# Optimization experiments

Measured on AMD Instinct MI355X. Metric: run time of the kernel, lower is better.

Reference implementation:

```python
import jax, jax.numpy as jnp
import numpy as np

SENSOR_H, SENSOR_W = 256, 256
SPP = 16
BATCH, C, H_IMG, W_IMG = 4, 3, 1024, 1024


def setup_inputs() -> dict:
    key = jax.random.key(0)
    k1, k2 = jax.random.split(key)
    img = jax.random.uniform(k1, (BATCH, C, H_IMG, W_IMG), dtype=jnp.float32)
    jitter = jax.random.uniform(k2, (SPP, SENSOR_H, SENSOR_W, 2), dtype=jnp.float32)
    t = jnp.ones((1,), jnp.float32)
    return {"img": img, "t": t, "jitter": jitter}


def deform(pos, t):
    # Analytic per-axis foveation diffeomorphism [-1,1]^2 -> [-1,1]^2:
    #   f(u) = tanh(t*u)/tanh(t), f'(u) = t*(1 - tanh(t*u)^2)/tanh(t)
    # Jacobian is diagonal, so det = f'(x) * f'(y).
    tt = t[0]
    s = jnp.tanh(tt)
    th = jnp.tanh(tt * pos)
    warped = th / s                      # (..., 2)
    dd = tt * (1.0 - th * th) / s        # diagonal Jacobian entries (..., 2)
    det = dd[..., 0] * dd[..., 1]        # (...)
    return warped, det


def grid_sample_border(img, grid):
    # img: (b,c,H,W); grid: (spp,h,w,2) in [-1,1]
    # bilinear, padding_mode='border', align_corners=False (matches F.grid_sample)
    b, c, H, W = img.shape
    gx = (grid[..., 0] + 1.0) * (W / 2.0) - 0.5
    gy = (grid[..., 1] + 1.0) * (H / 2.0) - 0.5
    gx = jnp.clip(gx, 0.0, W - 1.0)
    gy = jnp.clip(gy, 0.0, H - 1.0)
    x0 = jnp.floor(gx)
    y0 = jnp.floor(gy)
    wx = (gx - x0)[None, None]           # (1,1,spp,h,w)
    wy = (gy - y0)[None, None]
    x0i = jnp.clip(x0.astype(jnp.int32), 0, W - 1)
    y0i = jnp.clip(y0.astype(jnp.int32), 0, H - 1)
    x1i = jnp.clip(x0i + 1, 0, W - 1)
    y1i = jnp.clip(y0i + 1, 0, H - 1)
    # fancy-index gather: result (b,c,spp,h,w); avoids tiling img over (b*spp)
    v00 = img[:, :, y0i, x0i]
    v01 = img[:, :, y0i, x1i]
    v10 = img[:, :, y1i, x0i]
    v11 = img[:, :, y1i, x1i]
    return (v00 * (1 - wx) * (1 - wy) + v01 * wx * (1 - wy)
            + v10 * (1 - wx) * wy + v11 * wx * wy)


def reference(img, t, jitter):
    step_x = 2.0 / SENSOR_W
    step_y = 2.0 / SENSOR_H
    px = jnp.arange(-1.0, 1.0, step_x, dtype=jnp.float32)
    py = jnp.arange(-1.0, 1.0, step_y, dtype=jnp.float32)
    gx, gy = jnp.meshgrid(px, py, indexing='xy')          # (h, w)
    pixel_pos = jnp.stack((gx, gy), axis=-1)[None]        # (1, h, w, 2)
    jit = jitter * jnp.array([step_x, step_y], jnp.float32)
    pos = pixel_pos + jit                                 # (spp, h, w, 2)
    warped, det = deform(pos, t)                          # (spp,h,w,2), (spp,h,w)
    samples = grid_sample_border(img, warped)             # (b, c, spp, h, w)
    weighted = jnp.mean(samples * det[None, None], axis=2)  # (b, c, h, w)
    area = jnp.mean(det, axis=0)[None, None]              # (1, 1, h, w)
    return weighted / area
```

## Files before the change

kernel.cpp:

```cpp
#include <hip/hip_runtime.h>

#define SPP   16
#define SH    256
#define SW    256
#define HI    1024
#define WI    1024
#define CH    3
#define BATCH 4

__device__ __forceinline__ float fast_tanh(float x) {
    const float e = __expf(2.0f * x);
    return (e - 1.0f) * __builtin_amdgcn_rcpf(e + 1.0f);
}

__global__ __launch_bounds__(256) void foveated_batch(
    const float* __restrict__ img,
    const float* __restrict__ t_ptr,
    const float* __restrict__ jitter,
    float* __restrict__ out)
{
    const int L   = (blockIdx.x & 7) * 512 + (blockIdx.x >> 3);
    const int sy  = L >> 4;
    const int sx0 = (L & 15) * 16;

    const int th  = threadIdx.x;
    const int sp  = th & 15;
    const int pxl = th >> 4;
    const int sx  = sx0 + pxl;

    const float step  = 2.0f / 256.0f;
    const float tt    = t_ptr[0];
    const float inv_s = __builtin_amdgcn_rcpf(fast_tanh(tt));

    const float2 j = ((const float2*)jitter)[sp * (SH * SW) + sy * SW + sx];
    const float posx = (-1.0f + sx * step) + j.x * step;
    const float posy = (-1.0f + sy * step) + j.y * step;

    const float thx = fast_tanh(tt * posx);
    const float thy = fast_tanh(tt * posy);
    const float ddx = tt * (1.0f - thx * thx) * inv_s;
    const float ddy = tt * (1.0f - thy * thy) * inv_s;
    const float det = ddx * ddy;

    float gx = (thx * inv_s + 1.0f) * (WI * 0.5f) - 0.5f;
    float gy = (thy * inv_s + 1.0f) * (HI * 0.5f) - 0.5f;
    gx = fminf(fmaxf(gx, 0.0f), (float)(WI - 1));
    gy = fminf(fmaxf(gy, 0.0f), (float)(HI - 1));

    const int xb = min((int)gx, WI - 2);
    const int yb = min((int)gy, HI - 2);
    const float fx = gx - (float)xb;
    const float fy = gy - (float)yb;

    const float w00 = (1.0f - fx) * (1.0f - fy) * det;
    const float w01 = fx * (1.0f - fy) * det;
    const float w10 = (1.0f - fx) * fy * det;
    const float w11 = fx * fy * det;

    const int i0 = yb * WI + xb;
    const int i1 = i0 + WI;
    const size_t plane = (size_t)HI * WI;

    float acc[BATCH][CH];
    #pragma unroll
    for (int b = 0; b < BATCH; ++b) {
        const float* __restrict__ pb = img + (size_t)(b * CH) * plane;
        #pragma unroll
        for (int c = 0; c < CH; ++c) {
            const float* __restrict__ p = pb + c * plane;
            const float2 a = *(const float2*)(p + i0);
            const float2 d = *(const float2*)(p + i1);
            acc[b][c] = a.x * w00 + a.y * w01 + d.x * w10 + d.y * w11;
        }
    }

    float dsum = det;
    #pragma unroll
    for (int m = 1; m < 16; m <<= 1) {
        #pragma unroll
        for (int b = 0; b < BATCH; ++b)
            #pragma unroll
            for (int c = 0; c < CH; ++c)
                acc[b][c] += __shfl_xor(acc[b][c], m);
        dsum += __shfl_xor(dsum, m);
    }

    if (sp == 0) {
        const float inv_d = 1.0f / dsum;
        const int pix = sy * SW + sx;
        #pragma unroll
        for (int b = 0; b < BATCH; ++b)
            #pragma unroll
            for (int c = 0; c < CH; ++c)
                out[(size_t)(b * CH + c) * (SH * SW) + pix] = acc[b][c] * inv_d;
    }
}

extern "C" void kernel_launch(void* const* d_in, const int* in_sizes, int n_in,
                              void* d_out, int out_size, void* d_ws, size_t ws_size,
                              hipStream_t stream) {
    const float* img    = (const float*)d_in[0];
    const float* t      = (const float*)d_in[1];
    const float* jitter = (const float*)d_in[2];
    float* out          = (float*)d_out;

    hipLaunchKernelGGL(foveated_batch, dim3(4096), dim3(256), 0, stream,
                       img, t, jitter, out);
}
```

Baseline: 113.0 us.

## Stage per-tile image footprint in LDS as fp16 and process four samples per thread

Each block now covers a 16x4 sensor tile, computes the warped image bounding box, and cooperatively loads the footprint for all three channels of each batch into shared memory packed as half precision. Each thread handles four jitter samples and gathers bilinear taps from LDS, with a global-memory fallback when the footprint exceeds the buffer. The aim is fewer scattered global gathers, since overlapping taps are now reused. In exchange it adds block barriers, a serial batch loop, and reduced input precision from fp16 storage.

```diff
diff --git a/kernel.cpp b/kernel.cpp
--- a/kernel.cpp
+++ b/kernel.cpp
@@ -1,4 +1,5 @@
 #include <hip/hip_runtime.h>
+#include <hip/hip_fp16.h>
 
 #define SPP   16
 #define SH    256
@@ -8,75 +9,165 @@
 #define CH    3
 #define BATCH 4
 
+#define TSX   16
+#define TSY   4
+#define MAXW  92
+#define MAXH  26
+
 __device__ __forceinline__ float fast_tanh(float x) {
     const float e = __expf(2.0f * x);
     return (e - 1.0f) * __builtin_amdgcn_rcpf(e + 1.0f);
 }
 
-__global__ __launch_bounds__(256) void foveated_batch(
+__global__ __launch_bounds__(256) void foveated_tile4(
     const float* __restrict__ img,
     const float* __restrict__ t_ptr,
     const float* __restrict__ jitter,
     float* __restrict__ out)
 {
-    const int L   = (blockIdx.x & 7) * 512 + (blockIdx.x >> 3);
-    const int sy  = L >> 4;
-    const int sx0 = (L & 15) * 16;
-
-    const int th  = threadIdx.x;
-    const int sp  = th & 15;
-    const int pxl = th >> 4;
-    const int sx  = sx0 + pxl;
+    __shared__ uint2 lds[MAXH * MAXW];
+
+    const int bid = blockIdx.x;
+    const int L   = (bid & 7) * 128 + (bid >> 3);
+    const int ty  = L & 63;
+    const int tx  = L >> 6;
+
+    const int th = threadIdx.x;
+    const int lx = th & 15;
+    const int q  = (th >> 4) & 3;
+    const int ly = th >> 6;
+
+    const int sx = tx * TSX + lx;
+    const int sy = ty * TSY + ly;
 
     const float step  = 2.0f / 256.0f;
     const float tt    = t_ptr[0];
     const float inv_s = __builtin_amdgcn_rcpf(fast_tanh(tt));
 
-    const float2 j = ((const float2*)jitter)[sp * (SH * SW) + sy * SW + sx];
-    const float posx = (-1.0f + sx * step) + j.x * step;
-    const float posy = (-1.0f + sy * step) + j.y * step;
-
-    const float thx = fast_tanh(tt * posx);
-    const float thy = fast_tanh(tt * posy);
-    const float ddx = tt * (1.0f - thx * thx) * inv_s;
-    const float ddy = tt * (1.0f - thy * thy) * inv_s;
-    const float det = ddx * ddy;
-
-    float gx = (thx * inv_s + 1.0f) * (WI * 0.5f) - 0.5f;
-    float gy = (thy * inv_s + 1.0f) * (HI * 0.5f) - 0.5f;
-    gx = fminf(fmaxf(gx, 0.0f), (float)(WI - 1));
-    gy = fminf(fmaxf(gy, 0.0f), (float)(HI - 1));
-
-    const int xb = min((int)gx, WI - 2);
-    const int yb = min((int)gy, HI - 2);
-    const float fx = gx - (float)xb;
-    const float fy = gy - (float)yb;
-
-    const float w00 = (1.0f - fx) * (1.0f - fy) * det;
-    const float w01 = fx * (1.0f - fy) * det;
-    const float w10 = (1.0f - fx) * fy * det;
-    const float w11 = fx * fy * det;
-
-    const int i0 = yb * WI + xb;
-    const int i1 = i0 + WI;
+    auto gmap = [&](float p) {
+        float g = (fast_tanh(tt * p) * inv_s + 1.0f) * 512.0f - 0.5f;
+        return fminf(fmaxf(g, 0.0f), 1023.0f);
+    };
+    const float pxmin = -1.0f + (tx * TSX) * step, pxmax = pxmin + TSX * step;
+    const float pymin = -1.0f + (ty * TSY) * step, pymax = pymin + TSY * step;
+    const int x_lo = max((int)gmap(pxmin) - 1, 0);
+    const int x_hi = min((int)gmap(pxmax) + 2, WI - 1);
+    const int y_lo = max((int)gmap(pymin) - 1, 0);
+    const int y_hi = min((int)gmap(pymax) + 2, HI - 1);
+    const int ncols = x_hi - x_lo + 1;
+    const int nrows = y_hi - y_lo + 1;
+    const bool fits = (ncols <= MAXW) && (nrows <= MAXH);
+
+    float w00[4], w01[4], w10[4], w11[4];
+    int   li[4], gi[4];
+    float dsum = 0.0f;
+    const float2* __restrict__ jit2 = (const float2*)jitter;
+    const int jbase = sy * SW + sx;
+    const float px = -1.0f + sx * step;
+    const float py = -1.0f + sy * step;
+
+    #pragma unroll
+    for (int k = 0; k < 4; ++k) {
+        const int sp = q * 4 + k;
+        const float2 j = jit2[sp * (SH * SW) + jbase];
+        const float posx = px + j.x * step;
+        const float posy = py + j.y * step;
+
+        const float thx = fast_tanh(tt * posx);
+        const float thy = fast_tanh(tt * posy);
+        const float ddx = tt * (1.0f - thx * thx) * inv_s;
+        const float ddy = tt * (1.0f - thy * thy) * inv_s;
+        const float det = ddx * ddy;
+
+        float gx = (thx * inv_s + 1.0f) * (WI * 0.5f) - 0.5f;
+        float gy = (thy * inv_s + 1.0f) * (HI * 0.5f) - 0.5f;
+        gx = fminf(fmaxf(gx, 0.0f), (float)(WI - 1));
+        gy = fminf(fmaxf(gy, 0.0f), (float)(HI - 1));
+
+        const int xb = min((int)gx, WI - 2);
+        const int yb = min((int)gy, HI - 2);
+        const float fx = gx - (float)xb;
+        const float fy = gy - (float)yb;
+
+        w00[k] = (1.0f - fx) * (1.0f - fy) * det;
+        w01[k] = fx * (1.0f - fy) * det;
+        w10[k] = (1.0f - fx) * fy * det;
+        w11[k] = fx * fy * det;
+        dsum  += det;
+        li[k]  = (yb - y_lo) * MAXW + (xb - x_lo);
+        gi[k]  = yb * WI + xb;
+    }
+
     const size_t plane = (size_t)HI * WI;
-
     float acc[BATCH][CH];
     #pragma unroll
+    for (int b = 0; b < BATCH; ++b)
+        #pragma unroll
+        for (int c = 0; c < CH; ++c) acc[b][c] = 0.0f;
+
+    const int npix = nrows * ncols;
+    const unsigned mdiv = (1u << 22) / (unsigned)ncols + 1u;
+
+    #pragma unroll 1
     for (int b = 0; b < BATCH; ++b) {
-        const float* __restrict__ pb = img + (size_t)(b * CH) * plane;
-        #pragma unroll
-        for (int c = 0; c < CH; ++c) {
-            const float* __restrict__ p = pb + c * plane;
-            const float2 a = *(const float2*)(p + i0);
-            const float2 d = *(const float2*)(p + i1);
-            acc[b][c] = a.x * w00 + a.y * w01 + d.x * w10 + d.y * w11;
+        const float* __restrict__ p0 = img + (size_t)(b * CH) * plane;
+        const float* __restrict__ p1 = p0 + plane;
+        const float* __restrict__ p2 = p1 + plane;
+
+        if (fits) {
+            __syncthreads();
+            #pragma unroll
+            for (int it = 0; it < 10; ++it) {
+                const int idx = th + it * 256;
+                const int ii  = min(idx, npix - 1);
+                const int r   = (int)(((unsigned)ii * mdiv) >> 22);
+                const int c   = ii - r * ncols;
+                const int g   = (y_lo + r) * WI + (x_lo + c);
+                union { __half2 h[2]; uint2 u; } v;
+                v.h[0] = __floats2half2_rn(p0[g], p1[g]);
+                v.h[1] = __floats2half2_rn(p2[g], 0.0f);
+                if (idx < npix) lds[r * MAXW + c] = v.u;
+            }
+            __syncthreads();
+
+            #pragma unroll
+            for (int k = 0; k < 4; ++k) {
+                const int base = li[k];
+                const uint2 q00 = lds[base];
+                const uint2 q01 = lds[base + 1];
+                const uint2 q10 = lds[base + MAXW];
+                const uint2 q11 = lds[base + MAXW + 1];
+
+                const float2 a00 = __half22float2(*(const __half2*)&q00.x);
+                const float2 b00 = __half22float2(*(const __half2*)&q00.y);
+                const float2 a01 = __half22float2(*(const __half2*)&q01.x);
+                const float2 b01 = __half22float2(*(const __half2*)&q01.y);
+                const float2 a10 = __half22float2(*(const __half2*)&q10.x);
+                const float2 b10 = __half22float2(*(const __half2*)&q10.y);
+                const float2 a11 = __half22float2(*(const __half2*)&q11.x);
+                const float2 b11 = __half22float2(*(const __half2*)&q11.y);
+
+                acc[b][0] += w00[k]*a00.x + w01[k]*a01.x + w10[k]*a10.x + w11[k]*a11.x;
+                acc[b][1] += w00[k]*a00.y + w01[k]*a01.y + w10[k]*a10.y + w11[k]*a11.y;
+                acc[b][2] += w00[k]*b00.x + w01[k]*b01.x + w10[k]*b10.x + w11[k]*b11.x;
+            }
+        } else {
+            #pragma unroll
+            for (int k = 0; k < 4; ++k) {
+                const int i0 = gi[k];
+                const int i1 = i0 + WI;
+                { const float2 a = *(const float2*)(p0 + i0), d = *(const float2*)(p0 + i1);
+                  acc[b][0] += a.x*w00[k] + a.y*w01[k] + d.x*w10[k] + d.y*w11[k]; }
+                { const float2 a = *(const float2*)(p1 + i0), d = *(const float2*)(p1 + i1);
+                  acc[b][1] += a.x*w00[k] + a.y*w01[k] + d.x*w10[k] + d.y*w11[k]; }
+                { const float2 a = *(const float2*)(p2 + i0), d = *(const float2*)(p2 + i1);
+                  acc[b][2] += a.x*w00[k] + a.y*w01[k] + d.x*w10[k] + d.y*w11[k]; }
+            }
         }
     }
 
-    float dsum = det;
     #pragma unroll
-    for (int m = 1; m < 16; m <<= 1) {
+    for (int m = 16; m <= 32; m <<= 1) {
         #pragma unroll
         for (int b = 0; b < BATCH; ++b)
             #pragma unroll
@@ -85,7 +176,7 @@
         dsum += __shfl_xor(dsum, m);
     }
 
-    if (sp == 0) {
+    if (q == 0) {
         const float inv_d = 1.0f / dsum;
         const int pix = sy * SW + sx;
         #pragma unroll
@@ -104,6 +195,6 @@
     const float* jitter = (const float*)d_in[2];
     float* out          = (float*)d_out;
 
-    hipLaunchKernelGGL(foveated_batch, dim3(4096), dim3(256), 0, stream,
+    hipLaunchKernelGGL(foveated_tile4, dim3(1024), dim3(256), 0, stream,
                        img, t, jitter, out);
 }
```

Result: no change. 113.4 us (+0.3%).

## Repack image into interleaved fp16 pixel records and gather with half2 FMA

Applied to the files above, without the earlier changes.

Adds a pre-pass that packs the 12 batch/channel planes into one 32-byte fp16 record per pixel in the workspace. The main kernel then fetches each bilinear corner with a single contiguous load instead of 12 scattered plane loads. Each thread now handles 4 samples and accumulates in half2 FMAs. This trades an extra full-image read/write pass and fp16 precision loss, including fp16 accumulation of weighted sums, for far fewer cache lines touched per gather. It falls back to the old kernel if the workspace is too small.

```diff
diff --git a/kernel.cpp b/kernel.cpp
--- a/kernel.cpp
+++ b/kernel.cpp
@@ -1,16 +1,154 @@
 #include <hip/hip_runtime.h>
-
-#define SPP   16
-#define SH    256
-#define SW    256
-#define HI    1024
-#define WI    1024
-#define CH    3
-#define BATCH 4
+#include <hip/hip_fp16.h>
+
+#define SPP    16
+#define SH     256
+#define SW     256
+#define HI     1024
+#define WI     1024
+#define CH     3
+#define BATCH  4
+#define NPLANE (BATCH * CH)
+#define PXB    32
 
 __device__ __forceinline__ float fast_tanh(float x) {
     const float e = __expf(2.0f * x);
     return (e - 1.0f) * __builtin_amdgcn_rcpf(e + 1.0f);
+}
+
+__global__ __launch_bounds__(256) void repack12(
+    const float* __restrict__ img, char* __restrict__ dst)
+{
+    const int pix = blockIdx.x * 256 + threadIdx.x;
+    float v[NPLANE];
+    #pragma unroll
+    for (int p = 0; p < NPLANE; ++p)
+        v[p] = img[(size_t)p * (HI * WI) + pix];
+    union { __half2 h[6]; struct { uint4 a; uint2 b; } u; } o;
+    #pragma unroll
+    for (int i = 0; i < 6; ++i)
+        o.h[i] = __floats2half2_rn(v[2 * i], v[2 * i + 1]);
+    char* d = dst + (size_t)pix * PXB;
+    *(uint4*)d        = o.u.a;
+    *(uint2*)(d + 16) = o.u.b;
+}
+
+__global__ __launch_bounds__(256) void foveated_pk(
+    const char* __restrict__ pk,
+    const float* __restrict__ t_ptr,
+    const float* __restrict__ jitter,
+    float* __restrict__ out)
+{
+    const int L   = (blockIdx.x & 7) * 128 + (blockIdx.x >> 3);
+    const int th  = threadIdx.x;
+    const int lpx = th & 15;
+    const int q   = (th >> 4) & 3;
+    const int wv  = th >> 6;
+    const int pix = L * 64 + wv * 16 + lpx;
+    const int sx  = pix & (SW - 1);
+    const int sy  = pix >> 8;
+
+    const float step  = 2.0f / 256.0f;
+    const float tt    = t_ptr[0];
+    const float inv_s = __builtin_amdgcn_rcpf(fast_tanh(tt));
+    const float px    = -1.0f + sx * step;
+    const float py    = -1.0f + sy * step;
+
+    const float2* __restrict__ jit2 = (const float2*)jitter;
+
+    __half2 acc[6];
+    #pragma unroll
+    for (int i = 0; i < 6; ++i) acc[i] = __float2half2_rn(0.0f);
+    float dsum = 0.0f;
+
+    #pragma unroll
+    for (int k = 0; k < 4; ++k) {
+        const int sp = q * 4 + k;
+        const float2 j = jit2[sp * (SH * SW) + pix];
+        const float posx = px + j.x * step;
+        const float posy = py + j.y * step;
+
+        const float thx = fast_tanh(tt * posx);
+        const float thy = fast_tanh(tt * posy);
+        const float ddx = tt * (1.0f - thx * thx) * inv_s;
+        const float ddy = tt * (1.0f - thy * thy) * inv_s;
+        const float det = ddx * ddy;
+
+        float gx = (thx * inv_s + 1.0f) * (WI * 0.5f) - 0.5f;
+        float gy = (thy * inv_s + 1.0f) * (HI * 0.5f) - 0.5f;
+        gx = fminf(fmaxf(gx, 0.0f), (float)(WI - 1));
+        gy = fminf(fmaxf(gy, 0.0f), (float)(HI - 1));
+
+        const int xb = min((int)gx, WI - 2);
+        const int yb = min((int)gy, HI - 2);
+        const float fx = gx - (float)xb;
+        const float fy = gy - (float)yb;
+
+        const float w00 = (1.0f - fx) * (1.0f - fy) * det;
+        const float w01 = fx * (1.0f - fy) * det;
+        const float w10 = (1.0f - fx) * fy * det;
+        const float w11 = fx * fy * det;
+        dsum += det;
+
+        const __half2 W00 = __float2half2_rn(w00);
+        const __half2 W01 = __float2half2_rn(w01);
+        const __half2 W10 = __float2half2_rn(w10);
+        const __half2 W11 = __float2half2_rn(w11);
+
+        const char* r0 = pk + (size_t)((uint)(yb * WI + xb)) * PXB;
+        const char* r1 = r0 + WI * PXB;
+        const uint4 a0  = *(const uint4*)(r0);
+        const uint2 a0h = *(const uint2*)(r0 + 16);
+        const uint4 b0  = *(const uint4*)(r0 + PXB);
+        const uint2 b0h = *(const uint2*)(r0 + PXB + 16);
+        const uint4 a1  = *(const uint4*)(r1);
+        const uint2 a1h = *(const uint2*)(r1 + 16);
+        const uint4 b1  = *(const uint4*)(r1 + PXB);
+        const uint2 b1h = *(const uint2*)(r1 + PXB + 16);
+
+        const __half2* A0 = (const __half2*)&a0;
+        const __half2* B0 = (const __half2*)&b0;
+        const __half2* A1 = (const __half2*)&a1;
+        const __half2* B1 = (const __half2*)&b1;
+        #pragma unroll
+        for (int i = 0; i < 4; ++i) {
+            acc[i] = __hfma2(A0[i], W00, acc[i]);
+            acc[i] = __hfma2(B0[i], W01, acc[i]);
+            acc[i] = __hfma2(A1[i], W10, acc[i]);
+            acc[i] = __hfma2(B1[i], W11, acc[i]);
+        }
+        const __half2* A0H = (const __half2*)&a0h;
+        const __half2* B0H = (const __half2*)&b0h;
+        const __half2* A1H = (const __half2*)&a1h;
+        const __half2* B1H = (const __half2*)&b1h;
+        #pragma unroll
+        for (int i = 0; i < 2; ++i) {
+            acc[4 + i] = __hfma2(A0H[i], W00, acc[4 + i]);
+            acc[4 + i] = __hfma2(B0H[i], W01, acc[4 + i]);
+            acc[4 + i] = __hfma2(A1H[i], W10, acc[4 + i]);
+            acc[4 + i] = __hfma2(B1H[i], W11, acc[4 + i]);
+        }
+    }
+
+    #pragma unroll
+    for (int m = 16; m <= 32; m <<= 1) {
+        #pragma unroll
+        for (int i = 0; i < 6; ++i) {
+            const int t = __shfl_xor(__builtin_bit_cast(int, acc[i]), m);
+            acc[i] = __hadd2(acc[i], __builtin_bit_cast(__half2, t));
+        }
+        dsum += __shfl_xor(dsum, m);
+    }
+
+    if (q == 0) {
+        const float inv_d = 1.0f / dsum;
+        #pragma unroll
+        for (int p = 0; p < NPLANE; ++p) {
+            const float v = (p & 1) ? __high2float(acc[p >> 1])
+                                    : __low2float(acc[p >> 1]);
+            out[(size_t)p * (SH * SW) + pix] = v * inv_d;
+        }
+    }
 }
 
 __global__ __launch_bounds__(256) void foveated_batch(
@@ -22,7 +160,6 @@
     const int L   = (blockIdx.x & 7) * 512 + (blockIdx.x >> 3);
     const int sy  = L >> 4;
     const int sx0 = (L & 15) * 16;
-
     const int th  = threadIdx.x;
     const int sp  = th & 15;
     const int pxl = th >> 4;
@@ -104,6 +241,15 @@
     const float* jitter = (const float*)d_in[2];
     float* out          = (float*)d_out;
 
-    hipLaunchKernelGGL(foveated_batch, dim3(4096), dim3(256), 0, stream,
-                       img, t, jitter, out);
-}
+    const size_t need = (size_t)HI * WI * PXB;
+    if (ws_size >= need) {
+        char* pk = (char*)d_ws;
+        hipLaunchKernelGGL(repack12, dim3(HI * WI / 256), dim3(256), 0, stream,
+                           img, pk);
+        hipLaunchKernelGGL(foveated_pk, dim3(1024), dim3(256), 0, stream,
+                           pk, t, jitter, out);
+    } else {
+        hipLaunchKernelGGL(foveated_batch, dim3(4096), dim3(256), 0, stream,
+                           img, t, jitter, out);
+    }
+}
```

New measurement: 120.2 us. +6.3%, slower.

## Split batch-channel planes across two blocks to cut registers and raise occupancy

Applied to the files above, without the earlier changes.

Each block now handles 16 pixels for half of the 12 batch-channel planes (6 planes) rather than all 12. The grid doubles and a launch-bounds occupancy hint is added. All gathers for the 6 planes are issued before any arithmetic, which keeps more loads in flight per thread and needs fewer registers. The cost is computing the warp and jitter loads twice per pixel, and each block's pixels now come from a different part of the image, which may change cache reuse.

```diff
diff --git a/kernel.cpp b/kernel.cpp
--- a/kernel.cpp
+++ b/kernel.cpp
@@ -13,26 +13,29 @@
     return (e - 1.0f) * __builtin_amdgcn_rcpf(e + 1.0f);
 }
 
-__global__ __launch_bounds__(256) void foveated_batch(
+__global__ __launch_bounds__(256, 6) void foveated_split(
     const float* __restrict__ img,
     const float* __restrict__ t_ptr,
     const float* __restrict__ jitter,
     float* __restrict__ out)
 {
-    const int L   = (blockIdx.x & 7) * 512 + (blockIdx.x >> 3);
-    const int sy  = L >> 4;
-    const int sx0 = (L & 15) * 16;
+    const int L   = (blockIdx.x & 7) * 1024 + (blockIdx.x >> 3);
+    const int bh  = L & 1;
+    const int grp = L >> 1;
 
     const int th  = threadIdx.x;
     const int sp  = th & 15;
-    const int pxl = th >> 4;
-    const int sx  = sx0 + pxl;
+    const int lpx = (th >> 4) & 3;
+    const int wv  = th >> 6;
+    const int pix = grp * 16 + wv * 4 + lpx;
+    const int sx  = pix & (SW - 1);
+    const int sy  = pix >> 8;
 
     const float step  = 2.0f / 256.0f;
     const float tt    = t_ptr[0];
     const float inv_s = __builtin_amdgcn_rcpf(fast_tanh(tt));
 
-    const float2 j = ((const float2*)jitter)[sp * (SH * SW) + sy * SW + sx];
+    const float2 j = ((const float2*)jitter)[sp * (SH * SW) + pix];
     const float posx = (-1.0f + sx * step) + j.x * step;
     const float posy = (-1.0f + sy * step) + j.y * step;
 
@@ -61,38 +64,33 @@
     const int i1 = i0 + WI;
     const size_t plane = (size_t)HI * WI;
 
-    float acc[BATCH][CH];
+    const float* __restrict__ pb = img + (size_t)(bh * 6) * plane;
+    float2 r0[6], r1[6];
     #pragma unroll
-    for (int b = 0; b < BATCH; ++b) {
-        const float* __restrict__ pb = img + (size_t)(b * CH) * plane;
-        #pragma unroll
-        for (int c = 0; c < CH; ++c) {
-            const float* __restrict__ p = pb + c * plane;
-            const float2 a = *(const float2*)(p + i0);
-            const float2 d = *(const float2*)(p + i1);
-            acc[b][c] = a.x * w00 + a.y * w01 + d.x * w10 + d.y * w11;
-        }
+    for (int p = 0; p < 6; ++p) {
+        r0[p] = *(const float2*)(pb + p * plane + i0);
+        r1[p] = *(const float2*)(pb + p * plane + i1);
     }
+
+    float acc[6];
+    #pragma unroll
+    for (int p = 0; p < 6; ++p)
+        acc[p] = r0[p].x * w00 + r0[p].y * w01 + r1[p].x * w10 + r1[p].y * w11;
 
     float dsum = det;
     #pragma unroll
     for (int m = 1; m < 16; m <<= 1) {
         #pragma unroll
-        for (int b = 0; b < BATCH; ++b)
-            #pragma unroll
-            for (int c = 0; c < CH; ++c)
-                acc[b][c] += __shfl_xor(acc[b][c], m);
+        for (int p = 0; p < 6; ++p)
+            acc[p] += __shfl_xor(acc[p], m);
         dsum += __shfl_xor(dsum, m);
     }
 
     if (sp == 0) {
         const float inv_d = 1.0f / dsum;
-        const int pix = sy * SW + sx;
         #pragma unroll
-        for (int b = 0; b < BATCH; ++b)
-            #pragma unroll
-            for (int c = 0; c < CH; ++c)
-                out[(size_t)(b * CH + c) * (SH * SW) + pix] = acc[b][c] * inv_d;
+        for (int p = 0; p < 6; ++p)
+            out[(size_t)(bh * 6 + p) * (SH * SW) + pix] = acc[p] * inv_d;
     }
 }
 
@@ -104,6 +102,6 @@
     const float* jitter = (const float*)d_in[2];
     float* out          = (float*)d_out;
 
-    hipLaunchKernelGGL(foveated_batch, dim3(4096), dim3(256), 0, stream,
+    hipLaunchKernelGGL(foveated_split, dim3(8192), dim3(256), 0, stream,
                        img, t, jitter, out);
 }
```

New measurement: 114.4 us. About the same (+1.2%).
